# Kernel tuning notes

Measured on AMD Instinct MI355X. Metric: run time of the kernel, lower is better.

The kernel has to match this reference:

```python
import jax, jax.numpy as jnp
import numpy as np

B, T, D_IN, H, D_ENC, P, D_ATT = 64, 20, 512, 512, 2048, 196, 512


def setup_inputs() -> dict:
    key = jax.random.key(0)
    ks = jax.random.split(key, 12)
    s = 0.05  # weight scale to keep gates out of saturation
    return {
        "x": jax.random.normal(ks[0], (B, T, D_IN), jnp.float32),
        "cnn_features": jax.random.normal(ks[1], (B, P, D_ENC), jnp.float32),
        "Wi": jax.random.normal(ks[2], (D_IN + H + D_ENC, H), jnp.float32) * s,
        "bi": jnp.zeros((H,), jnp.float32),
        "Wf": jax.random.normal(ks[3], (D_IN + H + D_ENC, H), jnp.float32) * s,
        "bf": jnp.zeros((H,), jnp.float32),
        "Wc": jax.random.normal(ks[4], (D_IN + H + D_ENC, H), jnp.float32) * s,
        "bc": jnp.zeros((H,), jnp.float32),
        "Wo": jax.random.normal(ks[5], (D_IN + H + D_ENC, H), jnp.float32) * s,
        "bo": jnp.zeros((H,), jnp.float32),
        "Wa_feat": jax.random.normal(ks[6], (D_ENC, D_ATT), jnp.float32) * s,
        "Wa_h": jax.random.normal(ks[7], (H, D_ATT), jnp.float32) * s,
        "ba": jnp.zeros((D_ATT,), jnp.float32),
        "v": jax.random.normal(ks[8], (D_ATT,), jnp.float32) * s,
    }


def reference(x, cnn_features, Wi, bi, Wf, bf, Wc, bc, Wo, bo, Wa_feat, Wa_h, ba, v):
    batch, seq_len, _ = x.shape
    hid = Wi.shape[1]
    # feature projection is h-independent: hoist out of the time loop
    feat_proj = jnp.einsum('bpe,ea->bpa', cnn_features, Wa_feat) + ba  # [B,P,A]

    def step(carry, x_t):
        h, c = carry
        # additive (Bahdanau) attention over pixels
        e = jnp.einsum('bpa,a->bp', jnp.tanh(feat_proj + (h @ Wa_h)[:, None, :]), v)
        alpha = jax.nn.softmax(e, axis=-1)                      # [B,P]
        ctx = jnp.einsum('bp,bpe->be', alpha, cnn_features)     # [B,E]
        comb = jnp.concatenate([x_t, h, ctx], axis=1)           # [B,D_IN+H+E]
        i_t = jax.nn.sigmoid(comb @ Wi + bi)
        f_t = jax.nn.sigmoid(comb @ Wf + bf)
        o_t = jax.nn.sigmoid(comb @ Wo + bo)
        c_tilde = jnp.tanh(comb @ Wc + bc)
        c_new = f_t * c + i_t * c_tilde
        h_new = o_t * jnp.tanh(c_new)
        return (h_new, c_new), h_new

    h0 = jnp.zeros((batch, hid), x.dtype)
    c0 = jnp.zeros((batch, hid), x.dtype)
    (h_T, c_T), ys = jax.lax.scan(step, (h0, c0), jnp.swapaxes(x, 0, 1))
    outputs = jnp.swapaxes(ys, 0, 1)  # [B,T,H]
    return outputs, h_T, c_T
```

## Files before the change

### kernel.cpp

```cpp
#include <hip/hip_runtime.h>

typedef unsigned short u16;
typedef unsigned int u32;
typedef __attribute__((ext_vector_type(8))) short bf16x8;
typedef __attribute__((ext_vector_type(4))) float f32x4;

#define NB 64
#define NT 20
#define NH 512
#define NP 196
#define NE 2048
#define NA 512

__device__ __forceinline__ u16 f2bf(float f) {
  u32 b = __float_as_uint(f);
  return (u16)((b + 0x7FFFu + ((b >> 16) & 1u)) >> 16);
}
__device__ __forceinline__ float bf2f(u16 u) { return __uint_as_float(((u32)u) << 16); }
__device__ __forceinline__ float tanh_fast(float x) {
  float xc = fminf(fmaxf(x, -15.f), 15.f);
  float e2 = __builtin_amdgcn_exp2f(xc * 2.885390082f);
  return (e2 - 1.f) * __builtin_amdgcn_rcpf(e2 + 1.f);
}
__device__ __forceinline__ float sigmoid_fast(float x) {
  return __builtin_amdgcn_rcpf(1.f + __builtin_amdgcn_exp2f(x * -1.44269504f));
}

__device__ __forceinline__ void gload_lds16(const u16* g, u16* l) {
  __builtin_amdgcn_global_load_lds((const __attribute__((address_space(1))) void*)g,
                                   (__attribute__((address_space(3))) void*)l, 16, 0, 0);
}

template <int N>
__device__ __forceinline__ void vwait() {
  if constexpr (N >= 0)
    asm volatile("s_waitcnt vmcnt(%0)" ::"i"(N) : "memory");
  else
    asm volatile("" ::: "memory");
}

__global__ __launch_bounds__(256) void conv_bf16(const float4* __restrict__ src,
                                                 u16* __restrict__ dst, int n4) {
  int i = blockIdx.x * 256 + threadIdx.x;
  int stride = gridDim.x * 256;
  for (; i < n4; i += stride) {
    float4 v = src[i];
    u32 lo = (u32)f2bf(v.x) | ((u32)f2bf(v.y) << 16);
    u32 hi = (u32)f2bf(v.z) | ((u32)f2bf(v.w) << 16);
    *(uint2*)(dst + (size_t)i * 4) = make_uint2(lo, hi);
  }
}

__global__ __launch_bounds__(128) void conv_x(const float* __restrict__ x,
                                              u16* __restrict__ xbT) {
  int b = blockIdx.x, t = blockIdx.y, tid = threadIdx.x;
  float4 v = *(const float4*)(x + ((size_t)b * NT + t) * 512 + tid * 4);
  u32 lo = (u32)f2bf(v.x) | ((u32)f2bf(v.y) << 16);
  u32 hi = (u32)f2bf(v.z) | ((u32)f2bf(v.w) << 16);
  *(uint2*)(xbT + ((size_t)t * NB + b) * 512 + tid * 4) = make_uint2(lo, hi);
}

__global__ __launch_bounds__(256) void transpose_w(const float* __restrict__ W0,
                                                   const float* __restrict__ W1,
                                                   const float* __restrict__ W2,
                                                   const float* __restrict__ W3,
                                                   u16* __restrict__ dst, int row_off, int K) {
  const float* src = blockIdx.z == 0 ? W0 : blockIdx.z == 1 ? W1 : blockIdx.z == 2 ? W2 : W3;
  __shared__ float tile[32][33];
  int k0 = blockIdx.x * 32, n0 = blockIdx.y * 32;
  int tx = threadIdx.x & 31, ty = threadIdx.x >> 5;
#pragma unroll
  for (int i = 0; i < 4; ++i)
    tile[ty + i * 8][tx] = src[(size_t)(row_off + k0 + ty + i * 8) * 512 + n0 + tx];
  __syncthreads();
#pragma unroll
  for (int i = 0; i < 4; ++i) {
    int n = n0 + ty + i * 8, k = k0 + tx;
    dst[((size_t)blockIdx.z * 512 + n) * K + k] = f2bf(tile[tx][ty + i * 8]);
  }
}

__global__ __launch_bounds__(256) void gemm_bf16(const u16* __restrict__ A,
                                                 const u16* __restrict__ BT,
                                                 float* __restrict__ C, int M, int N, int K) {
  __shared__ u16 lA[128 * 64];
  __shared__ u16 lB[128 * 64];
  const int tid = threadIdx.x;
  const int lane = tid & 63;
  const int wid = tid >> 6;
  const int m0 = blockIdx.x * 128, n0 = blockIdx.y * 128;
  const int wm = (wid >> 1) * 64, wn = (wid & 1) * 64;
  f32x4 acc[4][4] = {};

  const int cbase = wid * 256;
  int srcr[4], srcc[4];
#pragma unroll
  for (int it = 0; it < 4; ++it) {
    int c = cbase + it * 64 + lane;
    srcr[it] = c >> 3;
    srcc[it] = ((c & 7) ^ ((c >> 3) & 7)) * 8;
  }

  for (int k0 = 0; k0 < K; k0 += 64) {
    __syncthreads();
#pragma unroll
    for (int it = 0; it < 4; ++it) {
      gload_lds16(A + (size_t)(m0 + srcr[it]) * K + k0 + srcc[it],
                  lA + (size_t)(cbase + it * 64) * 8);
      gload_lds16(BT + (size_t)(n0 + srcr[it]) * K + k0 + srcc[it],
                  lB + (size_t)(cbase + it * 64) * 8);
    }
    __syncthreads();
#pragma unroll
    for (int kk = 0; kk < 2; ++kk) {
      int kchunk = kk * 4 + (lane >> 4);
      bf16x8 af[4], bg[4];
#pragma unroll
      for (int i = 0; i < 4; ++i) {
        int row = wm + i * 16 + (lane & 15);
        af[i] = *(const bf16x8*)(lA + row * 64 + ((kchunk ^ (row & 7)) * 8));
        int rowb = wn + i * 16 + (lane & 15);
        bg[i] = *(const bf16x8*)(lB + rowb * 64 + ((kchunk ^ (rowb & 7)) * 8));
      }
#pragma unroll
      for (int i = 0; i < 4; ++i)
#pragma unroll
        for (int j = 0; j < 4; ++j)
          acc[i][j] = __builtin_amdgcn_mfma_f32_16x16x32_bf16(af[i], bg[j], acc[i][j], 0, 0, 0);
    }
  }
#pragma unroll
  for (int i = 0; i < 4; ++i) {
    int m = m0 + wm + i * 16 + ((lane >> 4) * 4);
#pragma unroll
    for (int j = 0; j < 4; ++j) {
      int n = n0 + wn + j * 16 + (lane & 15);
#pragma unroll
      for (int r = 0; r < 4; ++r) C[(size_t)(m + r) * N + n] = acc[i][j][r];
    }
  }
}

#define PHASE(MH, NH, CUR, DOSTAGE, MATB, HH, K1, WN)                                     \
  do {                                                                                    \
    const u16* pA_ = lds + (CUR) * 32768;                                                 \
    const u16* pB_ = pA_ + 16384;                                                         \
    bf16x8 af_[2][4], bg_[2][2];                                                          \
    _Pragma("unroll") for (int kh_ = 0; kh_ < 2; ++kh_) {                                 \
      const int kc_ = kh_ * 4 + (lane >> 4);                                              \
      _Pragma("unroll") for (int i_ = 0; i_ < 4; ++i_) {                                  \
        const int rw_ = (MH) * 128 + wmB + i_ * 16 + l15;                                 \
        af_[kh_][i_] = *(const bf16x8*)(pA_ + rw_ * 64 + ((kc_ ^ (rw_ & 7)) * 8));        \
      }                                                                                   \
      _Pragma("unroll") for (int j_ = 0; j_ < 2; ++j_) {                                  \
        const int rw_ = (NH) * 128 + wnB + j_ * 16 + l15;                                 \
        bg_[kh_][j_] = *(const bf16x8*)(pB_ + rw_ * 64 + ((kc_ ^ (rw_ & 7)) * 8));        \
      }                                                                                   \
    }                                                                                     \
    if (DOSTAGE) {                                                                        \
      const u16* gsrc_ = (MATB) ? BT : A;                                                 \
      const int r0_ = (MATB) ? n0 : m0;                                                   \
      u16* ldst_ = lds + (1 - (CUR)) * 32768 + (MATB) * 16384;                            \
      _Pragma("unroll") for (int s_ = 0; s_ < 2; ++s_)                                    \
          gload_lds16(gsrc_ + (size_t)(r0_ + srcR[HH][s_]) * K + (K1) + srcC[HH][s_],     \
                      ldst_ + ldsOff[HH][s_]);                                            \
    }                                                                                     \
    vwait<WN>();                                                                          \
    __builtin_amdgcn_s_barrier();                                                         \
    __builtin_amdgcn_s_setprio(1);                                                        \
    _Pragma("unroll") for (int kh_ = 0; kh_ < 2; ++kh_)                                   \
      _Pragma("unroll") for (int i_ = 0; i_ < 4; ++i_)                                    \
        _Pragma("unroll") for (int j_ = 0; j_ < 2; ++j_)                                  \
          acc[(MH) * 4 + i_][(NH) * 2 + j_] = __builtin_amdgcn_mfma_f32_16x16x32_bf16(    \
              af_[kh_][i_], bg_[kh_][j_], acc[(MH) * 4 + i_][(NH) * 2 + j_], 0, 0, 0);    \
    __builtin_amdgcn_s_setprio(0);                                                        \
    __builtin_amdgcn_s_barrier();                                                         \
  } while (0)

__global__ __launch_bounds__(512, 2) void gemm256(const u16* __restrict__ A,
                                                  const u16* __restrict__ BT,
                                                  const float* __restrict__ bias,
                                                  u16* __restrict__ fpb, u16* __restrict__ cnW,
                                                  int K, int grid_n) {
  __shared__ u16 lds[65536];
  const int tid = threadIdx.x;
  const int lane = tid & 63;
  const int wid = tid >> 6;
  const int l15 = lane & 15;
  const int nblk = gridDim.x;
  const int q = nblk >> 3, rr = nblk & 7;
  const int xcd = blockIdx.x & 7, jj = blockIdx.x >> 3;
  const int swz = (xcd < rr ? xcd * (q + 1) : rr * (q + 1) + (xcd - rr) * q) + jj;
  const int mt = swz / grid_n, nt = swz - mt * grid_n;
  const int m0 = mt * 256, n0 = nt * 256;
  const int wmB = (wid >> 2) * 64;
  const int wnB = (wid & 3) * 32;
  f32x4 acc[8][4] = {};

  int srcR[2][2], srcC[2][2], ldsOff[2][2];
#pragma unroll
  for (int h = 0; h < 2; ++h)
#pragma unroll
    for (int s = 0; s < 2; ++s) {
      int c = h * 1024 + s * 512 + wid * 64 + lane;
      srcR[h][s] = c >> 3;
      srcC[h][s] = ((c & 7) ^ ((c >> 3) & 7)) * 8;
      ldsOff[h][s] = (h * 1024 + s * 512 + wid * 64) * 8;
    }

#pragma unroll
  for (int s = 0; s < 2; ++s)
    gload_lds16(A + (size_t)(m0 + srcR[0][s]) * K + srcC[0][s], lds + ldsOff[0][s]);
#pragma unroll
  for (int s = 0; s < 2; ++s)
    gload_lds16(BT + (size_t)(n0 + srcR[0][s]) * K + srcC[0][s], lds + 16384 + ldsOff[0][s]);
#pragma unroll
  for (int s = 0; s < 2; ++s)
    gload_lds16(A + (size_t)(m0 + srcR[1][s]) * K + srcC[1][s], lds + ldsOff[1][s]);
#pragma unroll
  for (int s = 0; s < 2; ++s)
    gload_lds16(BT + (size_t)(n0 + srcR[1][s]) * K + srcC[1][s], lds + 16384 + ldsOff[1][s]);
  vwait<4>();
  __builtin_amdgcn_s_barrier();

  const int KT = K >> 6;
  for (int kt = 0; kt < KT - 1; ++kt) {
    const int cur = kt & 1;
    const int k1 = (kt + 1) << 6;
    PHASE(0, 0, cur, 1, 0, 0, k1, 4);
    PHASE(1, 0, cur, 1, 1, 0, k1, 4);
    PHASE(0, 1, cur, 1, 0, 1, k1, -1);
    PHASE(1, 1, cur, 1, 1, 1, k1, 4);
  }
  {
    const int cur = (KT - 1) & 1;
    PHASE(0, 0, cur, 0, 0, 0, 0, 2);
    PHASE(1, 0, cur, 0, 0, 0, 0, 0);
    PHASE(0, 1, cur, 0, 0, 0, 0, -1);
    PHASE(1, 1, cur, 0, 0, 0, 0, -1);
  }

#pragma unroll
  for (int i = 0; i < 8; ++i) {
    int m = m0 + (i >> 2) * 128 + wmB + (i & 3) * 16 + ((lane >> 4) * 4);
#pragma unroll
    for (int j = 0; j < 4; ++j) {
      int n = n0 + (j >> 1) * 128 + wnB + (j & 1) * 16 + l15;
      float bv = (n < 512) ? bias[n] : 0.f;
#pragma unroll
      for (int r = 0; r < 4; ++r) {
        float val = acc[i][j][r] + bv;
        u32 me = (u32)(m + r);
        if (n < 512) {
          fpb[(size_t)me * 512 + n] = f2bf(val);
        } else {
          u32 bdx = me / 196u;
          u32 p = me - bdx * 196u;
          u32 g = (u32)(n - 512) >> 9;
          u32 n9 = (u32)(n - 512) & 511u;
          cnW[(((size_t)bdx * 4 + g) * 196 + p) * 512 + n9] = f2bf(val);
        }
      }
    }
  }
}

__global__ __launch_bounds__(256) void hproj(const u16* __restrict__ hprev,
                                             const u16* __restrict__ wcT,
                                             float* __restrict__ hp) {
  const int ntile = blockIdx.x;
  const int tid = threadIdx.x, lane = tid & 63, kh = tid >> 6;
  const int l15 = lane & 15;
  const u16* Bp = wcT + (size_t)(ntile * 16 + l15) * 512 + kh * 128 + ((lane >> 4) * 8);
  const u16* Ap = hprev + (size_t)l15 * 512 + kh * 128 + ((lane >> 4) * 8);
  f32x4 acc[4] = {};
#pragma unroll
  for (int ks = 0; ks < 4; ++ks) {
    bf16x8 bb = *(const bf16x8*)(Bp + ks * 32);
#pragma unroll
    for (int mf = 0; mf < 4; ++mf) {
      bf16x8 a = *(const bf16x8*)(Ap + (size_t)mf * 16 * 512 + ks * 32);
      acc[mf] = __builtin_amdgcn_mfma_f32_16x16x32_bf16(a, bb, acc[mf], 0, 0, 0);
    }
  }
  __shared__ float pre[4][64][16];
  const int rrow = (lane >> 4) * 4;
#pragma unroll
  for (int mf = 0; mf < 4; ++mf)
#pragma unroll
    for (int r = 0; r < 4; ++r) pre[kh][mf * 16 + rrow + r][l15] = acc[mf][r];
  __syncthreads();
  const int m = tid >> 2, n = (tid & 3) * 4;
  float4 s;
  float* sp = (float*)&s;
#pragma unroll
  for (int j = 0; j < 4; ++j)
    sp[j] = pre[0][m][n + j] + pre[1][m][n + j] + pre[2][m][n + j] + pre[3][m][n + j];
  *(float4*)(hp + (size_t)m * 2560 + ntile * 16 + n) = s;
}

__global__ __launch_bounds__(1024) void attn_gates(
    const u16* __restrict__ fpb, const float* __restrict__ hp, const float* __restrict__ v,
    const u16* __restrict__ cw, const float* __restrict__ xw, const float* __restrict__ bi,
    const float* __restrict__ bfg, const float* __restrict__ bc, const float* __restrict__ bo,
    float* __restrict__ cbuf, float* __restrict__ out, u16* __restrict__ hnext, int t) {
  const int b = blockIdx.x & 63;
  const int half = blockIdx.x >> 6;
  const int tid = threadIdx.x;
  const int lane = tid & 63, wid = tid >> 6;
  __shared__ float smem_a[1024];
  __shared__ float sm[16];
  __shared__ float alp[200];
  __shared__ float red[8192];

  float* hwa = smem_a;
  float* vv = smem_a + 512;
  if (tid < 512) {
    hwa[tid] = (t > 0) ? hp[(size_t)b * 2560 + 2048 + tid] : 0.f;
    vv[tid] = v[tid];
  }
  if (tid >= 196 && tid < 256) red[tid] = -3e38f;
  __syncthreads();

  float hw[8], vr[8];
#pragma unroll
  for (int j = 0; j < 8; ++j) {
    hw[j] = hwa[lane * 8 + j];
    vr[j] = vv[lane * 8 + j];
  }
  for (int p = wid; p < NP; p += 16) {
    const u16* fp = fpb + ((size_t)b * NP + p) * 512 + lane * 8;
    uint4 raw = *(const uint4*)fp;
    u32 w[4] = {raw.x, raw.y, raw.z, raw.w};
    float part = 0.f;
#pragma unroll
    for (int j = 0; j < 8; ++j) {
      u16 u = (u16)(w[j >> 1] >> ((j & 1) * 16));
      part += tanh_fast(bf2f(u) + hw[j]) * vr[j];
    }
#pragma unroll
    for (int off = 32; off > 0; off >>= 1) part += __shfl_xor(part, off);
    if (lane == 0) red[p] = part;
  }
  __syncthreads();

  float ev = 0.f, w = 0.f;
  if (tid < 256) {
    ev = red[tid];
    float m_ = ev;
#pragma unroll
    for (int off = 32; off > 0; off >>= 1) m_ = fmaxf(m_, __shfl_xor(m_, off));
    if (lane == 0) sm[wid] = m_;
  }
  __syncthreads();
  if (tid < 256) {
    float mx = fmaxf(fmaxf(sm[0], sm[1]), fmaxf(sm[2], sm[3]));
    w = (tid < NP) ? __builtin_amdgcn_exp2f((ev - mx) * 1.44269504f) : 0.f;
    float s_ = w;
#pragma unroll
    for (int off = 32; off > 0; off >>= 1) s_ += __shfl_xor(s_, off);
    if (lane == 0) sm[8 + wid] = s_;
  }
  __syncthreads();
  if (tid < NP) {
    float tot = (sm[8] + sm[9]) + (sm[10] + sm[11]);
    alp[tid] = w * __builtin_amdgcn_rcpf(tot);
  }
  __syncthreads();

  {
    const int g = tid >> 8, pg = (tid >> 5) & 7, colc = tid & 31;
    const u16* base = cw + ((size_t)(b * 4 + g) * 196) * 512 + half * 256 + colc * 8;
    float acc[8] = {};
    for (int i = 0; i < 25; ++i) {
      int p = pg + i * 8;
      if (p < NP) {
        float al = alp[p];
        uint4 raw = *(const uint4*)(base + (size_t)p * 512);
        u32 wds[4] = {raw.x, raw.y, raw.z, raw.w};
#pragma unroll
        for (int j = 0; j < 8; ++j) acc[j] += al * bf2f((u16)(wds[j >> 1] >> ((j & 1) * 16)));
      }
    }
#pragma unroll
    for (int j = 0; j < 8; ++j) red[((g * 8 + pg) * 32 + colc) * 8 + j] = acc[j];
  }
  __syncthreads();

  float* pre4 = smem_a;
  {
    const int g = tid >> 8, nn = tid & 255;
    float s = 0.f;
#pragma unroll
    for (int pg = 0; pg < 8; ++pg) s += red[((g * 8 + pg) * 32 + (nn >> 3)) * 8 + (nn & 7)];
    pre4[g * 256 + nn] = s;
  }
  __syncthreads();

  if (tid < 256) {
    const int ng = half * 256 + tid;
    const size_t xwo = ((size_t)t * NB + b) * 2048;
    const size_t hpb = (size_t)b * 2560;
    float hwh0 = 0.f, hwh1 = 0.f, hwh2 = 0.f, hwh3 = 0.f;
    if (t > 0) {
      hwh0 = hp[hpb + ng];
      hwh1 = hp[hpb + 512 + ng];
      hwh2 = hp[hpb + 1024 + ng];
      hwh3 = hp[hpb + 1536 + ng];
    }
    float ip = pre4[0 * 256 + tid] + xw[xwo + ng] + hwh0 + bi[ng];
    float fp = pre4[1 * 256 + tid] + xw[xwo + 512 + ng] + hwh1 + bfg[ng];
    float cp = pre4[2 * 256 + tid] + xw[xwo + 1024 + ng] + hwh2 + bc[ng];
    float op = pre4[3 * 256 + tid] + xw[xwo + 1536 + ng] + hwh3 + bo[ng];
    float it = sigmoid_fast(ip), ft = sigmoid_fast(fp), ot = sigmoid_fast(op);
    float ctl = tanh_fast(cp);
    float cold = (t > 0) ? cbuf[(size_t)b * 512 + ng] : 0.f;
    float cn = ft * cold + it * ctl;
    float hn = ot * tanh_fast(cn);
    cbuf[(size_t)b * 512 + ng] = cn;
    hnext[(size_t)b * 512 + ng] = f2bf(hn);
    out[((size_t)b * NT + t) * 512 + ng] = hn;
    if (t == NT - 1) {
      out[(size_t)NB * NT * 512 + (size_t)b * 512 + ng] = hn;
      out[(size_t)NB * NT * 512 + (size_t)NB * 512 + (size_t)b * 512 + ng] = cn;
    }
  }
}

extern "C" void kernel_launch(void* const* d_in, const int* in_sizes, int n_in, void* d_out,
                              int out_size, void* d_ws, size_t ws_size, hipStream_t stream) {
  const float* x = (const float*)d_in[0];
  const float* cnn = (const float*)d_in[1];
  const float* Wi = (const float*)d_in[2];
  const float* bi = (const float*)d_in[3];
  const float* Wf = (const float*)d_in[4];
  const float* bfv = (const float*)d_in[5];
  const float* Wc = (const float*)d_in[6];
  const float* bc = (const float*)d_in[7];
  const float* Wo = (const float*)d_in[8];
  const float* bo = (const float*)d_in[9];
  const float* Waf = (const float*)d_in[10];
  const float* Wah = (const float*)d_in[11];
  const float* ba = (const float*)d_in[12];
  const float* v = (const float*)d_in[13];
  float* out = (float*)d_out;

  char* base = (char*)d_ws;
  size_t off = 0;
  auto alloc = [&](size_t bytes) {
    char* r = base + off;
    off += (bytes + 255) & ~(size_t)255;
    return r;
  };
  u16* cnnb = (u16*)alloc((size_t)NB * NP * NE * 2);
  u16* fpb = (u16*)alloc((size_t)NB * NP * NA * 2);
  u16* cnW = (u16*)alloc((size_t)NB * 4 * NP * 512 * 2);
  u16* wbig = (u16*)alloc((size_t)2560 * 2048 * 2);
  u16* wcombT = (u16*)alloc((size_t)2560 * 512 * 2);
  u16* wxt = (u16*)alloc((size_t)4 * 512 * 512 * 2);
  u16* xbT = (u16*)alloc((size_t)NT * NB * 512 * 2);
  float* xw = (float*)alloc((size_t)NT * NB * 2048 * 4);
  u16* hbuf = (u16*)alloc((size_t)2 * NB * 512 * 2);
  float* cbuf = (float*)alloc((size_t)NB * 512 * 4);
  float* hp = (float*)alloc((size_t)NB * 2560 * 4);

  (void)ws_size;
  (void)in_sizes;
  (void)n_in;
  (void)out_size;

  conv_bf16<<<2048, 256, 0, stream>>>((const float4*)cnn, cnnb, (NB * NP * NE) / 4);
  conv_x<<<dim3(NB, NT), 128, 0, stream>>>(x, xbT);
  {
    dim3 g1(512 / 32, 16, 4);
    transpose_w<<<g1, 256, 0, stream>>>(Wi, Wf, Wc, Wo, wxt, 0, 512);
    dim3 g2(2048 / 32, 16, 1);
    transpose_w<<<g2, 256, 0, stream>>>(Waf, Waf, Waf, Waf, wbig, 0, 2048);
    dim3 g3(2048 / 32, 16, 4);
    transpose_w<<<g3, 256, 0, stream>>>(Wi, Wf, Wc, Wo, wbig + (size_t)512 * 2048, 1024, 2048);
    dim3 g4(512 / 32, 16, 4);
    transpose_w<<<g4, 256, 0, stream>>>(Wi, Wf, Wc, Wo, wcombT, 512, 512);
    dim3 g5(512 / 32, 16, 1);
    transpose_w<<<g5, 256, 0, stream>>>(Wah, Wah, Wah, Wah, wcombT + (size_t)2048 * 512, 0, 512);
  }

  gemm256<<<49 * 10, 512, 0, stream>>>(cnnb, wbig, ba, fpb, cnW, 2048, 10);

  {
    dim3 g(1280 / 128, 2048 / 128);
    gemm_bf16<<<g, 256, 0, stream>>>(xbT, wxt, xw, 1280, 2048, 512);
  }

  for (int t = 0; t < NT; ++t) {
    const u16* hprev = hbuf + (size_t)(t & 1) * NB * 512;
    u16* hnext = hbuf + (size_t)((t + 1) & 1) * NB * 512;
    if (t > 0) hproj<<<160, 256, 0, stream>>>(hprev, wcombT, hp);
    attn_gates<<<128, 1024, 0, stream>>>(fpb, hp, v, cnW, xw, bi, bfv, bc, bo, cbuf, out, hnext,
                                         t);
  }
}
```

Baseline: 694.3 us.

## Split attention-gate kernel into quarters and reuse GEMM fragments across phases

The per-step attention/gate kernel now launches 256 blocks instead of 128. Each block handles a quarter of the hidden units instead of a half, so more CUs share the context reduction. The cost is that each block recomputes the attention scores and softmax, which are now duplicated four times per batch element. Separately, the large GEMM's phase order is changed to a serpentine pattern so A or B register fragments are reused between consecutive phases, cutting LDS reads.

New measurement: 675.4 us. 2.7% less time.

```diff
diff --git a/kernel.cpp b/kernel.cpp
--- a/kernel.cpp
+++ b/kernel.cpp
@@ -141,20 +141,26 @@
   }
 }
 
-#define PHASE(MH, NH, CUR, DOSTAGE, MATB, HH, K1, WN)                                     \
+#define PHASE(MH, NH, LA, LB, CUR, DOSTAGE, MATB, HH, K1, WN)                             \
   do {                                                                                    \
     const u16* pA_ = lds + (CUR) * 32768;                                                 \
     const u16* pB_ = pA_ + 16384;                                                         \
-    bf16x8 af_[2][4], bg_[2][2];                                                          \
-    _Pragma("unroll") for (int kh_ = 0; kh_ < 2; ++kh_) {                                 \
-      const int kc_ = kh_ * 4 + (lane >> 4);                                              \
-      _Pragma("unroll") for (int i_ = 0; i_ < 4; ++i_) {                                  \
-        const int rw_ = (MH) * 128 + wmB + i_ * 16 + l15;                                 \
-        af_[kh_][i_] = *(const bf16x8*)(pA_ + rw_ * 64 + ((kc_ ^ (rw_ & 7)) * 8));        \
+    if (LA) {                                                                             \
+      _Pragma("unroll") for (int kh_ = 0; kh_ < 2; ++kh_) {                               \
+        const int kc_ = kh_ * 4 + (lane >> 4);                                            \
+        _Pragma("unroll") for (int i_ = 0; i_ < 4; ++i_) {                                \
+          const int rw_ = (MH) * 128 + wmB + i_ * 16 + l15;                               \
+          af[kh_][i_] = *(const bf16x8*)(pA_ + rw_ * 64 + ((kc_ ^ (rw_ & 7)) * 8));       \
+        }                                                                                 \
       }                                                                                   \
-      _Pragma("unroll") for (int j_ = 0; j_ < 2; ++j_) {                                  \
-        const int rw_ = (NH) * 128 + wnB + j_ * 16 + l15;                                 \
-        bg_[kh_][j_] = *(const bf16x8*)(pB_ + rw_ * 64 + ((kc_ ^ (rw_ & 7)) * 8));        \
+    }                                                                                     \
+    if (LB) {                                                                             \
+      _Pragma("unroll") for (int kh_ = 0; kh_ < 2; ++kh_) {                               \
+        const int kc_ = kh_ * 4 + (lane >> 4);                                            \
+        _Pragma("unroll") for (int j_ = 0; j_ < 2; ++j_) {                                \
+          const int rw_ = (NH) * 128 + wnB + j_ * 16 + l15;                               \
+          bg[kh_][j_] = *(const bf16x8*)(pB_ + rw_ * 64 + ((kc_ ^ (rw_ & 7)) * 8));       \
+        }                                                                                 \
       }                                                                                   \
     }                                                                                     \
     if (DOSTAGE) {                                                                        \
@@ -172,7 +178,7 @@
       _Pragma("unroll") for (int i_ = 0; i_ < 4; ++i_)                                    \
         _Pragma("unroll") for (int j_ = 0; j_ < 2; ++j_)                                  \
           acc[(MH) * 4 + i_][(NH) * 2 + j_] = __builtin_amdgcn_mfma_f32_16x16x32_bf16(    \
-              af_[kh_][i_], bg_[kh_][j_], acc[(MH) * 4 + i_][(NH) * 2 + j_], 0, 0, 0);    \
+              af[kh_][i_], bg[kh_][j_], acc[(MH) * 4 + i_][(NH) * 2 + j_], 0, 0, 0);      \
     __builtin_amdgcn_s_setprio(0);                                                        \
     __builtin_amdgcn_s_barrier();                                                         \
   } while (0)
@@ -196,6 +202,7 @@
   const int wmB = (wid >> 2) * 64;
   const int wnB = (wid & 3) * 32;
   f32x4 acc[8][4] = {};
+  bf16x8 af[2][4], bg[2][2];
 
   int srcR[2][2], srcC[2][2], ldsOff[2][2];
 #pragma unroll
@@ -227,17 +234,17 @@
   for (int kt = 0; kt < KT - 1; ++kt) {
     const int cur = kt & 1;
     const int k1 = (kt + 1) << 6;
-    PHASE(0, 0, cur, 1, 0, 0, k1, 4);
-    PHASE(1, 0, cur, 1, 1, 0, k1, 4);
-    PHASE(0, 1, cur, 1, 0, 1, k1, -1);
-    PHASE(1, 1, cur, 1, 1, 1, k1, 4);
+    PHASE(0, 0, 1, 1, cur, 1, 0, 0, k1, 4);
+    PHASE(1, 0, 1, 0, cur, 1, 1, 0, k1, 4);
+    PHASE(1, 1, 0, 1, cur, 1, 0, 1, k1, -1);
+    PHASE(0, 1, 1, 0, cur, 1, 1, 1, k1, 4);
   }
   {
     const int cur = (KT - 1) & 1;
-    PHASE(0, 0, cur, 0, 0, 0, 0, 2);
-    PHASE(1, 0, cur, 0, 0, 0, 0, 0);
-    PHASE(0, 1, cur, 0, 0, 0, 0, -1);
-    PHASE(1, 1, cur, 0, 0, 0, 0, -1);
+    PHASE(0, 0, 1, 1, cur, 0, 0, 0, 0, 2);
+    PHASE(1, 0, 1, 0, cur, 0, 0, 0, 0, 0);
+    PHASE(1, 1, 0, 1, cur, 0, 0, 0, 0, -1);
+    PHASE(0, 1, 1, 0, cur, 0, 0, 0, 0, -1);
   }
 
 #pragma unroll
@@ -305,7 +312,7 @@
     const float* __restrict__ bfg, const float* __restrict__ bc, const float* __restrict__ bo,
     float* __restrict__ cbuf, float* __restrict__ out, u16* __restrict__ hnext, int t) {
   const int b = blockIdx.x & 63;
-  const int half = blockIdx.x >> 6;
+  const int quarter = blockIdx.x >> 6;
   const int tid = threadIdx.x;
   const int lane = tid & 63, wid = tid >> 6;
   __shared__ float smem_a[1024];
@@ -369,11 +376,11 @@
   __syncthreads();
 
   {
-    const int g = tid >> 8, pg = (tid >> 5) & 7, colc = tid & 31;
-    const u16* base = cw + ((size_t)(b * 4 + g) * 196) * 512 + half * 256 + colc * 8;
+    const int g = tid >> 8, pg = (tid >> 4) & 15, colc = tid & 15;
+    const u16* base = cw + ((size_t)(b * 4 + g) * 196) * 512 + quarter * 128 + colc * 8;
     float acc[8] = {};
-    for (int i = 0; i < 25; ++i) {
-      int p = pg + i * 8;
+    for (int i = 0; i < 13; ++i) {
+      int p = pg + i * 16;
       if (p < NP) {
         float al = alp[p];
         uint4 raw = *(const uint4*)(base + (size_t)p * 512);
@@ -383,22 +390,22 @@
       }
     }
 #pragma unroll
-    for (int j = 0; j < 8; ++j) red[((g * 8 + pg) * 32 + colc) * 8 + j] = acc[j];
+    for (int j = 0; j < 8; ++j) red[((g * 16 + pg) * 16 + colc) * 8 + j] = acc[j];
   }
   __syncthreads();
 
   float* pre4 = smem_a;
-  {
-    const int g = tid >> 8, nn = tid & 255;
+  if (tid < 512) {
+    const int g = tid >> 7, nn = tid & 127;
     float s = 0.f;
 #pragma unroll
-    for (int pg = 0; pg < 8; ++pg) s += red[((g * 8 + pg) * 32 + (nn >> 3)) * 8 + (nn & 7)];
-    pre4[g * 256 + nn] = s;
-  }
-  __syncthreads();
-
-  if (tid < 256) {
-    const int ng = half * 256 + tid;
+    for (int pg = 0; pg < 16; ++pg) s += red[((g * 16 + pg) * 16 + (nn >> 3)) * 8 + (nn & 7)];
+    pre4[g * 128 + nn] = s;
+  }
+  __syncthreads();
+
+  if (tid < 128) {
+    const int ng = quarter * 128 + tid;
     const size_t xwo = ((size_t)t * NB + b) * 2048;
     const size_t hpb = (size_t)b * 2560;
     float hwh0 = 0.f, hwh1 = 0.f, hwh2 = 0.f, hwh3 = 0.f;
@@ -408,10 +415,10 @@
       hwh2 = hp[hpb + 1024 + ng];
       hwh3 = hp[hpb + 1536 + ng];
     }
-    float ip = pre4[0 * 256 + tid] + xw[xwo + ng] + hwh0 + bi[ng];
-    float fp = pre4[1 * 256 + tid] + xw[xwo + 512 + ng] + hwh1 + bfg[ng];
-    float cp = pre4[2 * 256 + tid] + xw[xwo + 1024 + ng] + hwh2 + bc[ng];
-    float op = pre4[3 * 256 + tid] + xw[xwo + 1536 + ng] + hwh3 + bo[ng];
+    float ip = pre4[0 * 128 + tid] + xw[xwo + ng] + hwh0 + bi[ng];
+    float fp = pre4[1 * 128 + tid] + xw[xwo + 512 + ng] + hwh1 + bfg[ng];
+    float cp = pre4[2 * 128 + tid] + xw[xwo + 1024 + ng] + hwh2 + bc[ng];
+    float op = pre4[3 * 128 + tid] + xw[xwo + 1536 + ng] + hwh3 + bo[ng];
     float it = sigmoid_fast(ip), ft = sigmoid_fast(fp), ot = sigmoid_fast(op);
     float ctl = tanh_fast(cp);
     float cold = (t > 0) ? cbuf[(size_t)b * 512 + ng] : 0.f;
@@ -495,7 +502,7 @@
     const u16* hprev = hbuf + (size_t)(t & 1) * NB * 512;
     u16* hnext = hbuf + (size_t)((t + 1) & 1) * NB * 512;
     if (t > 0) hproj<<<160, 256, 0, stream>>>(hprev, wcombT, hp);
-    attn_gates<<<128, 1024, 0, stream>>>(fpb, hp, v, cnW, xw, bi, bfv, bc, bo, cbuf, out, hnext,
+    attn_gates<<<256, 1024, 0, stream>>>(fpb, hp, v, cnW, xw, bi, bfv, bc, bo, cbuf, out, hnext,
                                          t);
   }
 }
```
